# Kernel tuning notes

Hardware: AMD Instinct MI355X
Metric: run time of the kernel (lower is better)

## Reference

```python
import jax, jax.numpy as jnp
import numpy as np

MIN_NORM = 1e-5
C = 1.0
CLIP_R = 1.0

@jax.custom_vjp
def riemannian_grad_fix(x):
    # identity fwd; bwd rescales grad by the inverse conformal metric (hyptorch RiemannianGradient)
    return x

def _rgf_fwd(x):
    return x, x

def _rgf_bwd(x, g):
    scale = (1.0 - C * jnp.sum(x * x, axis=-1, keepdims=True)) ** 2 / 4.0
    return (g * scale,)

riemannian_grad_fix.defvjp(_rgf_fwd, _rgf_bwd)

def expmap0(u, c):
    sqrt_c = jnp.sqrt(c)
    u_norm = jnp.maximum(jnp.linalg.norm(u, axis=-1, keepdims=True), MIN_NORM)
    return jnp.tanh(sqrt_c * u_norm) * u / (sqrt_c * u_norm)

def project(x, c):
    norm = jnp.maximum(jnp.linalg.norm(x, axis=-1, keepdims=True), MIN_NORM)
    maxnorm = (1.0 - 1e-3) / jnp.sqrt(c)
    return jnp.where(norm > maxnorm, x / norm * maxnorm, x)

def to_poincare(x, c):
    # clip_r=1 clipping, then expmap0 + project; riemannian grad fix is identity in fwd
    x_norm = jnp.linalg.norm(x, axis=-1, keepdims=True) + 1e-5
    fac = jnp.minimum(jnp.ones_like(x_norm), CLIP_R / x_norm)
    x = x * fac
    return riemannian_grad_fix(project(expmap0(x, c), c))

def hyperbolic_softmax(X, A, P, c):
    # X: (B, d) points on the ball; A, P: (n, d)
    sqrt_c = jnp.sqrt(c)
    p2 = jnp.sum(P * P, axis=1)                       # (n,)
    a_norm = jnp.linalg.norm(A, axis=1)               # (n,)
    lam = 2.0 / (1.0 - c * p2)                        # (n,)
    k = lam * a_norm / sqrt_c                         # (n,)
    # batched mobius addition (-P) (+) X  -> (n, B, d)
    xy = jnp.einsum('nd,bd->nb', -P, X)               # (n, B)
    y2 = jnp.sum(X * X, axis=1)[None, :]              # (1, B)
    x2 = p2[:, None]                                  # (n, 1)
    num_coef = 1.0 + 2.0 * c * xy + c * y2            # (n, B)
    mob = num_coef[..., None] * (-P)[:, None, :] + (1.0 - c * x2)[..., None] * X[None, :, :]
    denom = 1.0 + 2.0 * c * xy + (c ** 2) * x2 * y2   # (n, B)
    mob = mob / (denom[..., None] + 1e-5)
    num = 2.0 * sqrt_c * jnp.einsum('nbd,nd->nb', mob, A)
    den = a_norm[:, None] * (1.0 - c * jnp.sum(mob * mob, axis=2))
    logit = k[:, None] * jnp.arcsinh(num / den)       # (n, B)
    return logit.T                                    # (B, n)

def setup_inputs() -> dict:
    key = jax.random.key(0)
    k1, k2, k3 = jax.random.split(key, 3)
    B, N, D = 2048, 512, 256
    x = jax.random.normal(k1, (B, D), dtype=jnp.float32)
    a_vals = jax.random.normal(k2, (N, D), dtype=jnp.float32) * 0.05
    p_vals = jax.random.normal(k3, (N, D), dtype=jnp.float32) * 0.05
    return {"x": x, "a_vals": a_vals, "p_vals": p_vals}

def reference(x, a_vals, p_vals):
    c = jnp.asarray(C, dtype=x.dtype)
    xb = to_poincare(x, c)
    p_poincare = expmap0(p_vals, c)                                   # (n, d)
    conformal = 1.0 - c * jnp.sum(p_poincare ** 2, axis=1, keepdims=True)  # (n, 1)
    a_poincare = a_vals * conformal                                   # (n, d)
    return hyperbolic_softmax(xb, a_poincare, p_poincare, c)          # (B, n)
```

## Files before the change

kernel.cpp:

```cpp
#include <hip/hip_runtime.h>
#include <math.h>

#define BB 2048
#define NN 512
#define DD 256

typedef __attribute__((ext_vector_type(8))) short s16x8;
typedef __attribute__((ext_vector_type(4))) float f32x4;

#define MFMA_BF16 __builtin_amdgcn_mfma_f32_16x16x32_bf16

__device__ __forceinline__ ushort f2bf(float f) {
    union { float f; unsigned u; } c; c.f = f;
    return (ushort)((c.u + 0x7fffu + ((c.u >> 16) & 1u)) >> 16);
}
__device__ __forceinline__ float bf2f(ushort h) {
    union { unsigned u; float f; } c; c.u = ((unsigned)h) << 16;
    return c.f;
}

__device__ __forceinline__ void split4(f32x4 v, float s, uint2* hi, uint2* lo) {
    float a = v.x * s, b = v.y * s, c = v.z * s, d = v.w * s;
    ushort ha = f2bf(a), hb = f2bf(b), hc = f2bf(c), hd = f2bf(d);
    ushort la = f2bf(a - bf2f(ha)), lb = f2bf(b - bf2f(hb));
    ushort lc = f2bf(c - bf2f(hc)), ld = f2bf(d - bf2f(hd));
    hi->x = (unsigned)ha | ((unsigned)hb << 16);
    hi->y = (unsigned)hc | ((unsigned)hd << 16);
    lo->x = (unsigned)la | ((unsigned)lb << 16);
    lo->y = (unsigned)lc | ((unsigned)ld << 16);
}

__device__ __forceinline__ float fast_asinh(float z) {
    float az = fabsf(z);
    float r = __logf(az + sqrtf(fmaf(az, az, 1.0f)));
    return copysignf(r, z);
}

__global__ __launch_bounds__(256) void hmlr_transform(
    const float* __restrict__ x, const float* __restrict__ a_vals,
    const float* __restrict__ p_vals,
    ushort* __restrict__ Xh, ushort* __restrict__ Xl,
    ushort* __restrict__ Ph, ushort* __restrict__ Pl,
    ushort* __restrict__ Ah, ushort* __restrict__ Al,
    float* __restrict__ y2, float* __restrict__ p2s, float* __restrict__ pas,
    float* __restrict__ ans, float* __restrict__ ks)
{
    const int lane = threadIdx.x & 63;
    const int wid  = blockIdx.x * 4 + (threadIdx.x >> 6);
    const int e0   = lane * 4;

    if (wid < BB) {
        const int r = wid;
        f32x4 v = *(const f32x4*)&x[(size_t)r * DD + e0];
        float ss = v.x * v.x + v.y * v.y + v.z * v.z + v.w * v.w;
        #pragma unroll
        for (int m = 32; m; m >>= 1) ss += __shfl_xor(ss, m, 64);
        float norm0 = sqrtf(ss);
        float fac = fminf(1.0f, 1.0f / (norm0 + 1e-5f));
        float u = fmaxf(norm0 * fac, 1e-5f);
        float th = tanhf(u);
        float en = fmaxf(th, 1e-5f);
        float wgt = (en > 0.999f) ? (0.999f / en) : 1.0f;
        float s = fac * (th / u) * wgt;
        if (lane == 0) { float fn = th * wgt; y2[r] = fn * fn; }
        uint2 hi, lo;
        split4(v, s, &hi, &lo);
        int es = e0 ^ ((r & 7) << 3);
        *(uint2*)&Xh[(size_t)r * DD + es] = hi;
        *(uint2*)&Xl[(size_t)r * DD + es] = lo;
    } else {
        const int n = wid - BB;
        f32x4 pv = *(const f32x4*)&p_vals[(size_t)n * DD + e0];
        f32x4 av = *(const f32x4*)&a_vals[(size_t)n * DD + e0];
        float sp = pv.x * pv.x + pv.y * pv.y + pv.z * pv.z + pv.w * pv.w;
        float sa = av.x * av.x + av.y * av.y + av.z * av.z + av.w * av.w;
        float sx = pv.x * av.x + pv.y * av.y + pv.z * av.z + pv.w * av.w;
        #pragma unroll
        for (int m = 32; m; m >>= 1) {
            sp += __shfl_xor(sp, m, 64);
            sa += __shfl_xor(sa, m, 64);
            sx += __shfl_xor(sx, m, 64);
        }
        float u = fmaxf(sqrtf(sp), 1e-5f);
        float th = tanhf(u);
        float spp = th / u;
        float p2 = th * th;
        float conf = 1.0f - p2;
        if (lane == 0) {
            p2s[n] = p2;
            pas[n] = spp * conf * sx;
            float an = sqrtf(sa) * conf;
            ans[n] = an;
            ks[n] = (2.0f / conf) * an;
        }
        int es = e0 ^ ((n & 7) << 3);
        uint2 hi, lo;
        split4(pv, spp, &hi, &lo);
        *(uint2*)&Ph[(size_t)n * DD + es] = hi;
        *(uint2*)&Pl[(size_t)n * DD + es] = lo;
        split4(av, conf, &hi, &lo);
        *(uint2*)&Ah[(size_t)n * DD + es] = hi;
        *(uint2*)&Al[(size_t)n * DD + es] = lo;
    }
}

__global__ __launch_bounds__(512) void hmlr_gemm(
    const ushort* __restrict__ Xh, const ushort* __restrict__ Xl,
    const ushort* __restrict__ Ph, const ushort* __restrict__ Pl,
    const ushort* __restrict__ Ah, const ushort* __restrict__ Al,
    const float* __restrict__ y2, const float* __restrict__ p2s,
    const float* __restrict__ pas, const float* __restrict__ ans,
    const float* __restrict__ ks, float* __restrict__ out)
{
    extern __shared__ ushort T[];

    const int t    = threadIdx.x;
    const int lane = t & 63;
    const int w    = t >> 6;
    const int bid  = blockIdx.x;
    const int xcd  = bid & 7;
    const int j    = bid >> 3;
    const int b0   = (xcd * 4 + (j >> 3)) * 64;
    const int n0   = (j & 7) * 64;
    const int wr   = w >> 2;
    const int wc   = w & 3;

    const ushort* bases[6] = {Xh, Xl, Ph, Pl, Ah, Al};

    f32x4 axy0 = {0.f,0.f,0.f,0.f}, axy1 = {0.f,0.f,0.f,0.f};
    f32x4 axa0 = {0.f,0.f,0.f,0.f}, axa1 = {0.f,0.f,0.f,0.f};

    auto stage = [&](int buf, int s) {
        #pragma unroll
        for (int i = 0; i < 6; ++i) {
            int g = w * 6 + i;
            int mat = g >> 3;
            int sub = g & 7;
            int grow = (mat < 2 ? b0 : n0) + sub * 8 + (lane >> 3);
            const ushort* src = bases[mat] + (size_t)grow * DD + s * 64 + (lane & 7) * 8;
            const ushort* dst = T + (((buf * 6 + mat) * 64 + sub * 8) * 64);
            __builtin_amdgcn_global_load_lds(
                (const __attribute__((address_space(1))) unsigned int*)(const void*)src,
                (__attribute__((address_space(3))) unsigned int*)(void*)dst,
                16, 0, 0);
        }
    };

    const int ram = wr * 32 + (lane & 15);
    const int rbn = wc * 16 + (lane & 15);
    const int gb  = (lane >> 4) << 4;

    stage(0, 0);

    const int n = n0 + rbn;
    float p2 = p2s[n], pa = pas[n], an = ans[n], kk = ks[n];
    float yv[8];
    #pragma unroll
    for (int m = 0; m < 2; ++m)
        #pragma unroll
        for (int rg = 0; rg < 4; ++rg)
            yv[m * 4 + rg] = y2[b0 + wr * 32 + m * 16 + (lane >> 4) * 4 + rg];
    asm volatile("" :: "v"(p2), "v"(pa), "v"(an), "v"(kk));
    #pragma unroll
    for (int i = 0; i < 8; ++i) asm volatile("" :: "v"(yv[i]));

    for (int s = 0; s < 4; ++s) {
        __syncthreads();
        if (s < 3) stage((s + 1) & 1, s + 1);
        const int bf = s & 1;
        #pragma unroll
        for (int ksl = 0; ksl < 2; ++ksl) {
            const int kb = ksl * 64 + gb;
            const ushort* base = T + (bf * 6 * 64 * 64);
            const char* x0 = (const char*)(base + (0 * 64 + ram) * 64);
            const char* x1 = (const char*)(base + (1 * 64 + ram) * 64);
            const int sa0 = kb ^ ((ram & 7) << 4);
            const int sb0 = kb ^ ((rbn & 7) << 4);
            const int sa1 = kb ^ (((ram + 16) & 7) << 4);
            s16x8 xh0 = *(const s16x8*)(x0 + sa0);
            s16x8 xh1 = *(const s16x8*)(x0 + 16 * 128 + sa1);
            s16x8 xl0 = *(const s16x8*)(x1 + sa0);
            s16x8 xl1 = *(const s16x8*)(x1 + 16 * 128 + sa1);
            s16x8 ph  = *(const s16x8*)((const char*)(base + (2 * 64 + rbn) * 64) + sb0);
            s16x8 pl  = *(const s16x8*)((const char*)(base + (3 * 64 + rbn) * 64) + sb0);
            s16x8 ah  = *(const s16x8*)((const char*)(base + (4 * 64 + rbn) * 64) + sb0);
            s16x8 al  = *(const s16x8*)((const char*)(base + (5 * 64 + rbn) * 64) + sb0);
            axy0 = MFMA_BF16(xh0, ph, axy0, 0, 0, 0);
            axy0 = MFMA_BF16(xh0, pl, axy0, 0, 0, 0);
            axy0 = MFMA_BF16(xl0, ph, axy0, 0, 0, 0);
            axy1 = MFMA_BF16(xh1, ph, axy1, 0, 0, 0);
            axy1 = MFMA_BF16(xh1, pl, axy1, 0, 0, 0);
            axy1 = MFMA_BF16(xl1, ph, axy1, 0, 0, 0);
            axa0 = MFMA_BF16(xh0, ah, axa0, 0, 0, 0);
            axa0 = MFMA_BF16(xh0, al, axa0, 0, 0, 0);
            axa0 = MFMA_BF16(xl0, ah, axa0, 0, 0, 0);
            axa1 = MFMA_BF16(xh1, ah, axa1, 0, 0, 0);
            axa1 = MFMA_BF16(xh1, al, axa1, 0, 0, 0);
            axa1 = MFMA_BF16(xl1, ah, axa1, 0, 0, 0);
        }
    }

    #pragma unroll
    for (int m = 0; m < 2; ++m) {
        f32x4 acc_xy = m ? axy1 : axy0;
        f32x4 acc_xa = m ? axa1 : axa0;
        #pragma unroll
        for (int rg = 0; rg < 4; ++rg) {
            int b = b0 + wr * 32 + m * 16 + (lane >> 4) * 4 + rg;
            float yy  = yv[m * 4 + rg];
            float xy  = -acc_xy[rg];
            float xa  =  acc_xa[rg];
            float dnm = 1.f + 2.f * xy + p2 * yy + 1e-5f;
            float alpha = (1.f + 2.f * xy + yy) / dnm;
            float beta  = (1.f - p2) / dnm;
            float num  = 2.f * (beta * xa - alpha * pa);
            float mob2 = alpha * alpha * p2 + beta * beta * yy
                       + 2.f * alpha * beta * xy;
            float den  = an * (1.f - mob2);
            out[(size_t)b * NN + n] = kk * fast_asinh(num / den);
        }
    }
}

extern "C" void kernel_launch(void* const* d_in, const int* in_sizes, int n_in,
                              void* d_out, int out_size, void* d_ws, size_t ws_size,
                              hipStream_t stream) {
    const float* x      = (const float*)d_in[0];
    const float* a_vals = (const float*)d_in[1];
    const float* p_vals = (const float*)d_in[2];
    float* out = (float*)d_out;

    ushort* Xh = (ushort*)d_ws;
    ushort* Xl = Xh + (size_t)BB * DD;
    ushort* Ph = Xl + (size_t)BB * DD;
    ushort* Pl = Ph + (size_t)NN * DD;
    ushort* Ah = Pl + (size_t)NN * DD;
    ushort* Al = Ah + (size_t)NN * DD;
    float*  y2  = (float*)(Al + (size_t)NN * DD);
    float*  p2s = y2 + BB;
    float*  pas = p2s + NN;
    float*  ans = pas + NN;
    float*  ks  = ans + NN;

    (void)hipFuncSetAttribute(reinterpret_cast<const void*>(hmlr_gemm),
                              hipFuncAttributeMaxDynamicSharedMemorySize, 98304);

    hipLaunchKernelGGL(hmlr_transform, dim3((BB + NN) / 4), dim3(256), 0, stream,
                       x, a_vals, p_vals, Xh, Xl, Ph, Pl, Ah, Al,
                       y2, p2s, pas, ans, ks);
    hipLaunchKernelGGL(hmlr_gemm, dim3(256), dim3(512), 98304, stream,
                       Xh, Xl, Ph, Pl, Ah, Al, y2, p2s, pas, ans, ks, out);
}
```

Before: 18.29 us.

## Replace split-bf16 GEMM with single fp16 MFMA and register-resident P/A operands

Drops the hi/lo bf16 split (three MFMAs per product) and uses one fp16 MFMA per product, so the transform writes half as much data and the GEMM does a third of the matrix work. The GEMM is restructured to 32x64 tiles over 512 blocks. All of K is loaded at once: X goes into a small static LDS buffer, while P and A rows are read straight into registers, which removes the double-buffered K loop and its barriers. The risk is accuracy: fp16 has fewer mantissa bits than the split-bf16 scheme, and the larger register footprint may affect occupancy.

```diff
diff --git a/kernel.cpp b/kernel.cpp
--- a/kernel.cpp
+++ b/kernel.cpp
@@ -5,31 +5,20 @@
 #define NN 512
 #define DD 256
 
-typedef __attribute__((ext_vector_type(8))) short s16x8;
+typedef __attribute__((ext_vector_type(8))) _Float16 f16x8;
 typedef __attribute__((ext_vector_type(4))) float f32x4;
 
-#define MFMA_BF16 __builtin_amdgcn_mfma_f32_16x16x32_bf16
+#define MFMA_F16 __builtin_amdgcn_mfma_f32_16x16x32_f16
 
-__device__ __forceinline__ ushort f2bf(float f) {
-    union { float f; unsigned u; } c; c.f = f;
-    return (ushort)((c.u + 0x7fffu + ((c.u >> 16) & 1u)) >> 16);
+__device__ __forceinline__ ushort f2h(float f) {
+    union { _Float16 h; ushort u; } c; c.h = (_Float16)f; return c.u;
 }
-__device__ __forceinline__ float bf2f(ushort h) {
-    union { unsigned u; float f; } c; c.u = ((unsigned)h) << 16;
-    return c.f;
+__device__ __forceinline__ uint2 pack4h(f32x4 v, float s) {
+    uint2 r;
+    r.x = (unsigned)f2h(v.x * s) | ((unsigned)f2h(v.y * s) << 16);
+    r.y = (unsigned)f2h(v.z * s) | ((unsigned)f2h(v.w * s) << 16);
+    return r;
 }
-
-__device__ __forceinline__ void split4(f32x4 v, float s, uint2* hi, uint2* lo) {
-    float a = v.x * s, b = v.y * s, c = v.z * s, d = v.w * s;
-    ushort ha = f2bf(a), hb = f2bf(b), hc = f2bf(c), hd = f2bf(d);
-    ushort la = f2bf(a - bf2f(ha)), lb = f2bf(b - bf2f(hb));
-    ushort lc = f2bf(c - bf2f(hc)), ld = f2bf(d - bf2f(hd));
-    hi->x = (unsigned)ha | ((unsigned)hb << 16);
-    hi->y = (unsigned)hc | ((unsigned)hd << 16);
-    lo->x = (unsigned)la | ((unsigned)lb << 16);
-    lo->y = (unsigned)lc | ((unsigned)ld << 16);
-}
-
 __device__ __forceinline__ float fast_asinh(float z) {
     float az = fabsf(z);
     float r = __logf(az + sqrtf(fmaf(az, az, 1.0f)));
@@ -39,9 +28,7 @@
 __global__ __launch_bounds__(256) void hmlr_transform(
     const float* __restrict__ x, const float* __restrict__ a_vals,
     const float* __restrict__ p_vals,
-    ushort* __restrict__ Xh, ushort* __restrict__ Xl,
-    ushort* __restrict__ Ph, ushort* __restrict__ Pl,
-    ushort* __restrict__ Ah, ushort* __restrict__ Al,
+    ushort* __restrict__ Xf, ushort* __restrict__ Pf, ushort* __restrict__ Af,
     float* __restrict__ y2, float* __restrict__ p2s, float* __restrict__ pas,
     float* __restrict__ ans, float* __restrict__ ks)
 {
@@ -63,11 +50,8 @@
         float wgt = (en > 0.999f) ? (0.999f / en) : 1.0f;
         float s = fac * (th / u) * wgt;
         if (lane == 0) { float fn = th * wgt; y2[r] = fn * fn; }
-        uint2 hi, lo;
-        split4(v, s, &hi, &lo);
         int es = e0 ^ ((r & 7) << 3);
-        *(uint2*)&Xh[(size_t)r * DD + es] = hi;
-        *(uint2*)&Xl[(size_t)r * DD + es] = lo;
+        *(uint2*)&Xf[(size_t)r * DD + es] = pack4h(v, s);
     } else {
         const int n = wid - BB;
         f32x4 pv = *(const f32x4*)&p_vals[(size_t)n * DD + e0];
@@ -93,26 +77,19 @@
             ans[n] = an;
             ks[n] = (2.0f / conf) * an;
         }
-        int es = e0 ^ ((n & 7) << 3);
-        uint2 hi, lo;
-        split4(pv, spp, &hi, &lo);
-        *(uint2*)&Ph[(size_t)n * DD + es] = hi;
-        *(uint2*)&Pl[(size_t)n * DD + es] = lo;
-        split4(av, conf, &hi, &lo);
-        *(uint2*)&Ah[(size_t)n * DD + es] = hi;
-        *(uint2*)&Al[(size_t)n * DD + es] = lo;
+        *(uint2*)&Pf[(size_t)n * DD + e0] = pack4h(pv, spp);
+        *(uint2*)&Af[(size_t)n * DD + e0] = pack4h(av, conf);
     }
 }
 
-__global__ __launch_bounds__(512) void hmlr_gemm(
-    const ushort* __restrict__ Xh, const ushort* __restrict__ Xl,
-    const ushort* __restrict__ Ph, const ushort* __restrict__ Pl,
-    const ushort* __restrict__ Ah, const ushort* __restrict__ Al,
+__global__ __launch_bounds__(512, 4) void hmlr_gemm(
+    const ushort* __restrict__ Xf, const ushort* __restrict__ Pf,
+    const ushort* __restrict__ Af,
     const float* __restrict__ y2, const float* __restrict__ p2s,
     const float* __restrict__ pas, const float* __restrict__ ans,
     const float* __restrict__ ks, float* __restrict__ out)
 {
-    extern __shared__ ushort T[];
+    __shared__ ushort Xs[32][256];
 
     const int t    = threadIdx.x;
     const int lane = t & 63;
@@ -120,105 +97,79 @@
     const int bid  = blockIdx.x;
     const int xcd  = bid & 7;
     const int j    = bid >> 3;
-    const int b0   = (xcd * 4 + (j >> 3)) * 64;
+    const int b0   = (xcd * 8 + (j >> 3)) * 32;
     const int n0   = (j & 7) * 64;
     const int wr   = w >> 2;
     const int wc   = w & 3;
+    const int ge   = (lane >> 4) * 8;
+    const int ram  = wr * 16 + (lane & 15);
+    const int rbn  = wc * 16 + (lane & 15);
 
-    const ushort* bases[6] = {Xh, Xl, Ph, Pl, Ah, Al};
-
-    f32x4 axy0 = {0.f,0.f,0.f,0.f}, axy1 = {0.f,0.f,0.f,0.f};
-    f32x4 axa0 = {0.f,0.f,0.f,0.f}, axa1 = {0.f,0.f,0.f,0.f};
-
-    auto stage = [&](int buf, int s) {
+    {
+        const int c = w * 2;
+        const ushort* src = Xf + (size_t)(b0 + c * 2 + (lane >> 5)) * DD + (lane & 31) * 8;
+        ushort* dst = &Xs[c * 2][0];
         #pragma unroll
-        for (int i = 0; i < 6; ++i) {
-            int g = w * 6 + i;
-            int mat = g >> 3;
-            int sub = g & 7;
-            int grow = (mat < 2 ? b0 : n0) + sub * 8 + (lane >> 3);
-            const ushort* src = bases[mat] + (size_t)grow * DD + s * 64 + (lane & 7) * 8;
-            const ushort* dst = T + (((buf * 6 + mat) * 64 + sub * 8) * 64);
+        for (int i = 0; i < 2; ++i) {
             __builtin_amdgcn_global_load_lds(
-                (const __attribute__((address_space(1))) unsigned int*)(const void*)src,
-                (__attribute__((address_space(3))) unsigned int*)(void*)dst,
+                (const __attribute__((address_space(1))) unsigned int*)(const void*)(src + i * 2 * DD),
+                (__attribute__((address_space(3))) unsigned int*)(void*)(dst + i * 2 * DD),
                 16, 0, 0);
         }
-    };
+    }
 
-    const int ram = wr * 32 + (lane & 15);
-    const int rbn = wc * 16 + (lane & 15);
-    const int gb  = (lane >> 4) << 4;
-
-    stage(0, 0);
+    const ushort* pr = Pf + (size_t)(n0 + rbn) * DD;
+    const ushort* ar = Af + (size_t)(n0 + rbn) * DD;
+    f16x8 pf[8], af[8];
+    #pragma unroll
+    for (int q = 0; q < 8; ++q) {
+        pf[q] = *(const f16x8*)(pr + q * 32 + ge);
+        af[q] = *(const f16x8*)(ar + q * 32 + ge);
+    }
 
     const int n = n0 + rbn;
     float p2 = p2s[n], pa = pas[n], an = ans[n], kk = ks[n];
-    float yv[8];
+    float yv[4];
     #pragma unroll
-    for (int m = 0; m < 2; ++m)
-        #pragma unroll
-        for (int rg = 0; rg < 4; ++rg)
-            yv[m * 4 + rg] = y2[b0 + wr * 32 + m * 16 + (lane >> 4) * 4 + rg];
+    for (int rg = 0; rg < 4; ++rg)
+        yv[rg] = y2[b0 + wr * 16 + (lane >> 4) * 4 + rg];
+
+    #pragma unroll
+    for (int q = 0; q < 8; ++q)
+        asm volatile("" :: "v"(pf[q]), "v"(af[q]));
     asm volatile("" :: "v"(p2), "v"(pa), "v"(an), "v"(kk));
     #pragma unroll
-    for (int i = 0; i < 8; ++i) asm volatile("" :: "v"(yv[i]));
+    for (int i = 0; i < 4; ++i) asm volatile("" :: "v"(yv[i]));
+    asm volatile("" ::: "memory");
 
-    for (int s = 0; s < 4; ++s) {
-        __syncthreads();
-        if (s < 3) stage((s + 1) & 1, s + 1);
-        const int bf = s & 1;
-        #pragma unroll
-        for (int ksl = 0; ksl < 2; ++ksl) {
-            const int kb = ksl * 64 + gb;
-            const ushort* base = T + (bf * 6 * 64 * 64);
-            const char* x0 = (const char*)(base + (0 * 64 + ram) * 64);
-            const char* x1 = (const char*)(base + (1 * 64 + ram) * 64);
-            const int sa0 = kb ^ ((ram & 7) << 4);
-            const int sb0 = kb ^ ((rbn & 7) << 4);
-            const int sa1 = kb ^ (((ram + 16) & 7) << 4);
-            s16x8 xh0 = *(const s16x8*)(x0 + sa0);
-            s16x8 xh1 = *(const s16x8*)(x0 + 16 * 128 + sa1);
-            s16x8 xl0 = *(const s16x8*)(x1 + sa0);
-            s16x8 xl1 = *(const s16x8*)(x1 + 16 * 128 + sa1);
-            s16x8 ph  = *(const s16x8*)((const char*)(base + (2 * 64 + rbn) * 64) + sb0);
-            s16x8 pl  = *(const s16x8*)((const char*)(base + (3 * 64 + rbn) * 64) + sb0);
-            s16x8 ah  = *(const s16x8*)((const char*)(base + (4 * 64 + rbn) * 64) + sb0);
-            s16x8 al  = *(const s16x8*)((const char*)(base + (5 * 64 + rbn) * 64) + sb0);
-            axy0 = MFMA_BF16(xh0, ph, axy0, 0, 0, 0);
-            axy0 = MFMA_BF16(xh0, pl, axy0, 0, 0, 0);
-            axy0 = MFMA_BF16(xl0, ph, axy0, 0, 0, 0);
-            axy1 = MFMA_BF16(xh1, ph, axy1, 0, 0, 0);
-            axy1 = MFMA_BF16(xh1, pl, axy1, 0, 0, 0);
-            axy1 = MFMA_BF16(xl1, ph, axy1, 0, 0, 0);
-            axa0 = MFMA_BF16(xh0, ah, axa0, 0, 0, 0);
-            axa0 = MFMA_BF16(xh0, al, axa0, 0, 0, 0);
-            axa0 = MFMA_BF16(xl0, ah, axa0, 0, 0, 0);
-            axa1 = MFMA_BF16(xh1, ah, axa1, 0, 0, 0);
-            axa1 = MFMA_BF16(xh1, al, axa1, 0, 0, 0);
-            axa1 = MFMA_BF16(xl1, ah, axa1, 0, 0, 0);
-        }
+    __syncthreads();
+
+    f32x4 axy = {0.f,0.f,0.f,0.f}, axa = {0.f,0.f,0.f,0.f};
+    const int swzA = (ram & 7) << 3;
+    const ushort* r0 = &Xs[ram][0];
+    #pragma unroll
+    for (int q = 0; q < 8; ++q) {
+        int f = q * 32 + ge;
+        int p = (f & ~63) | ((f & 63) ^ swzA);
+        f16x8 xf = *(const f16x8*)(r0 + p);
+        axy = MFMA_F16(xf, pf[q], axy, 0, 0, 0);
+        axa = MFMA_F16(xf, af[q], axa, 0, 0, 0);
     }
 
     #pragma unroll
-    for (int m = 0; m < 2; ++m) {
-        f32x4 acc_xy = m ? axy1 : axy0;
-        f32x4 acc_xa = m ? axa1 : axa0;
-        #pragma unroll
-        for (int rg = 0; rg < 4; ++rg) {
-            int b = b0 + wr * 32 + m * 16 + (lane >> 4) * 4 + rg;
-            float yy  = yv[m * 4 + rg];
-            float xy  = -acc_xy[rg];
-            float xa  =  acc_xa[rg];
-            float dnm = 1.f + 2.f * xy + p2 * yy + 1e-5f;
-            float alpha = (1.f + 2.f * xy + yy) / dnm;
-            float beta  = (1.f - p2) / dnm;
-            float num  = 2.f * (beta * xa - alpha * pa);
-            float mob2 = alpha * alpha * p2 + beta * beta * yy
-                       + 2.f * alpha * beta * xy;
-            float den  = an * (1.f - mob2);
-            out[(size_t)b * NN + n] = kk * fast_asinh(num / den);
-        }
+    for (int rg = 0; rg < 4; ++rg) {
+        int b = b0 + wr * 16 + (lane >> 4) * 4 + rg;
+        float yy  = yv[rg];
+        float xy  = -axy[rg];
+        float xa  =  axa[rg];
+        float dnm = 1.f + 2.f * xy + p2 * yy + 1e-5f;
+        float alpha = (1.f + 2.f * xy + yy) / dnm;
+        float beta  = (1.f - p2) / dnm;
+        float num  = 2.f * (beta * xa - alpha * pa);
+        float mob2 = alpha * alpha * p2 + beta * beta * yy
+                   + 2.f * alpha * beta * xy;
+        float den  = an * (1.f - mob2);
+        out[(size_t)b * NN + n] = kk * fast_asinh(num / den);
     }
 }
 
@@ -230,24 +181,17 @@
     const float* p_vals = (const float*)d_in[2];
     float* out = (float*)d_out;
 
-    ushort* Xh = (ushort*)d_ws;
-    ushort* Xl = Xh + (size_t)BB * DD;
-    ushort* Ph = Xl + (size_t)BB * DD;
-    ushort* Pl = Ph + (size_t)NN * DD;
-    ushort* Ah = Pl + (size_t)NN * DD;
-    ushort* Al = Ah + (size_t)NN * DD;
-    float*  y2  = (float*)(Al + (size_t)NN * DD);
+    ushort* Xf = (ushort*)d_ws;
+    ushort* Pf = Xf + (size_t)BB * DD;
+    ushort* Af = Pf + (size_t)NN * DD;
+    float*  y2  = (float*)(Af + (size_t)NN * DD);
     float*  p2s = y2 + BB;
     float*  pas = p2s + NN;
     float*  ans = pas + NN;
     float*  ks  = ans + NN;
 
-    (void)hipFuncSetAttribute(reinterpret_cast<const void*>(hmlr_gemm),
-                              hipFuncAttributeMaxDynamicSharedMemorySize, 98304);
-
     hipLaunchKernelGGL(hmlr_transform, dim3((BB + NN) / 4), dim3(256), 0, stream,
-                       x, a_vals, p_vals, Xh, Xl, Ph, Pl, Ah, Al,
-                       y2, p2s, pas, ans, ks);
-    hipLaunchKernelGGL(hmlr_gemm, dim3(256), dim3(512), 98304, stream,
-                       Xh, Xl, Ph, Pl, Ah, Al, y2, p2s, pas, ans, ks, out);
+                       x, a_vals, p_vals, Xf, Pf, Af, y2, p2s, pas, ans, ks);
+    hipLaunchKernelGGL(hmlr_gemm, dim3(512), dim3(512), 0, stream,
+                       Xf, Pf, Af, y2, p2s, pas, ans, ks, out);
 }
```

New measurement: 20.88 us. +14.2%, slower.
